# Optimization experiments

Measured on AMD Instinct MI355X. Metric: run time of the kernel, lower is better.

## Reference

```python
import jax, jax.numpy as jnp
import numpy as np

N_SIGMA = 1
K_INST = 8  # instance ids 1..K_INST (0 = background)
W_INST, W_VAR, W_SEED = 1.0, 10.0, 1.0
FG_WEIGHT = 1.0


def make_xym(h, w):
    # torch buffer: linspace(0,2,2048) x / linspace(0,1,1024) y, sliced to [0:h,0:w]
    xm = jnp.linspace(0.0, 2.0, 2048)[:w]
    ym = jnp.linspace(0.0, 1.0, 1024)[:h]
    return jnp.stack([jnp.broadcast_to(xm[None, :], (h, w)),
                      jnp.broadcast_to(ym[:, None], (h, w))], axis=0)  # [2,h,w]


def lovasz_hinge_flat(logits, labels):
    # logits, labels: [N] float (labels in {0,1})
    signs = 2.0 * labels - 1.0
    errors = 1.0 - logits * signs
    order = jnp.argsort(-errors)            # descending sort of errors
    errors_sorted = errors[order]
    gt_sorted = labels[order]
    gts = gt_sorted.sum()
    inter = gts - jnp.cumsum(gt_sorted)
    union = gts + jnp.cumsum(1.0 - gt_sorted)
    jac = 1.0 - inter / union
    grad = jnp.concatenate([jac[:1], jac[1:] - jac[:-1]])
    # torch impl wraps grad in Variable() -> no gradient through grad
    return jnp.dot(jax.nn.relu(errors_sorted), jax.lax.stop_gradient(grad))


def spatial_emb_loss(predictions, instances):
    B, C, T, h, w = predictions.shape
    xym = make_xym(h, w)
    # Faithful to the torch source: due to loop indentation, only the last
    # time step's var/instance/seed losses survive, and obj_count == 1.
    pred = predictions[:, :, T - 1]          # [B,C,h,w]
    inst = instances[:, 0, T - 1]            # [B,h,w] int
    spatial_emb = jnp.tanh(pred[:, 0:2]) + xym[None]   # [B,2,h,w]
    sigma = pred[:, 2:2 + N_SIGMA]                     # [B,1,h,w]
    seed = jax.nn.sigmoid(pred[:, 2 + N_SIGMA])        # [B,h,w]
    npix = float(h * w)

    def per_image(se, sig, sd, ins):
        bg_loss = jnp.sum(jnp.where(ins == 0, sd ** 2, 0.0))

        def per_id(k):
            m = (ins == k).astype(se.dtype)            # [h,w]
            cnt = m.sum()
            safe = jnp.maximum(cnt, 1.0)
            # to_center=True: center of in-mask pixel coordinates
            center = jnp.sum(xym * m[None], axis=(1, 2)) / safe      # [2]
            s_mean = jnp.sum(sig * m[None], axis=(1, 2)) / safe      # [n_sigma]
            var_l = jnp.sum(m[None] * (sig - jax.lax.stop_gradient(s_mean)[:, None, None]) ** 2) / (safe * N_SIGMA)
            s_exp = jnp.exp(s_mean * 10.0)
            dist = jnp.exp(-jnp.sum((se - center[:, None, None]) ** 2 * s_exp[:, None, None], axis=0))  # [h,w]
            inst_l = lovasz_hinge_flat((dist * 2.0 - 1.0).reshape(-1), m.reshape(-1))
            seed_l = FG_WEIGHT * jnp.sum(m * (sd - jax.lax.stop_gradient(dist)) ** 2)
            present = (cnt > 0).astype(se.dtype)       # torch skips absent ids
            return present * var_l, present * inst_l, present * seed_l

        var_l, inst_l, seed_l = jax.vmap(per_id)(jnp.arange(1, K_INST + 1))
        seed_loss = (bg_loss + seed_l.sum()) / npix
        # obj_count == 1 in the original code (incremented once per t-loop)
        return W_INST * inst_l.sum() + W_VAR * var_l.sum() + W_SEED * seed_loss

    per_b = jax.vmap(per_image)(spatial_emb, sigma, seed, inst)
    # torch: loss = loss / b, with b == B-1 after the loop
    return per_b.sum() / (B - 1)


def setup_inputs():
    key = jax.random.key(0)
    k1, k2 = jax.random.split(key)
    B, C, T, H, W = 4, 4, 2, 512, 1024
    predictions = jax.random.normal(k1, (B, C, T, H, W), dtype=jnp.float32)
    instances = jax.random.randint(k2, (B, 1, T, H, W), 0, K_INST + 1, dtype=jnp.int32)
    labels = jnp.zeros((B, 1, T, H, W), dtype=jnp.int32)  # unused by forward
    return {"predictions": predictions, "instances": instances, "labels": labels}


def reference(predictions, instances, labels):
    return spatial_emb_loss(predictions, instances)
```

## Files before the change

kernel.cpp:

```cpp
#include <hip/hip_runtime.h>

#define H 512
#define WID 1024
#define HW (H*WID)
#define B 4
#define K 8
#define NB 1024
#define NBLK1 128

#define OFF_LOSS  0
#define OFF_TICK  1
#define OFF_FIN   16
#define OFF_SPART 512
#define OFF_RED   (OFF_SPART + B*K*NBLK1*8)
#define OFF_PART  (OFF_RED + 2*B*K*NB)

static __device__ __forceinline__ float frcp(float x){
#if __has_builtin(__builtin_amdgcn_rcpf)
  return __builtin_amdgcn_rcpf(x);
#else
  return 1.0f / x;
#endif
}
static __device__ __forceinline__ float fexp2(float x){
#if __has_builtin(__builtin_amdgcn_exp2f)
  return __builtin_amdgcn_exp2f(x);
#else
  return exp2f(x);
#endif
}
static __device__ __forceinline__ float ftanh(float x){
  return 1.0f - 2.0f * frcp(__expf(2.0f*x) + 1.0f);
}
static __device__ __forceinline__ float fsigmoid(float x){
  return frcp(1.0f + __expf(-x));
}

__global__ __launch_bounds__(512) void k1_stats(const float* __restrict__ pred,
                                                const int* __restrict__ inst,
                                                float* __restrict__ ws) {
  const int b = blockIdx.y;
  __shared__ int4   ti[1024];
  __shared__ float4 ts[1024];
  __shared__ float  part5[K][5];
  const float4* sig4 = (const float4*)(pred + (size_t)(8*b + 5) * HW);
  const int4*   ins4 = (const int4*)(inst + (size_t)(2*b + 1) * HW);
  const int base4 = blockIdx.x * 1024;
  #pragma unroll
  for (int i = 0; i < 2; i++) {
    const int q = threadIdx.x + i*512;
    ti[q] = ins4[base4 + q];
    ts[q] = sig4[base4 + q];
  }
  __syncthreads();
  const int wv = threadIdx.x >> 6, lane = threadIdx.x & 63;
  const int kk = wv + 1;
  float cnt=0.f, sx=0.f, sy=0.f, ss=0.f, ss2=0.f;
  #pragma unroll
  for (int j = 0; j < 16; j++) {
    const int q = lane + 64*j;
    const int4   iv = ti[q];
    const float4 sv = ts[q];
    const int p = (base4 + q) * 4;
    const float xm0 = (float)(p & (WID-1)) * (2.0f/2047.0f);
    const float ym  = (float)(p >> 10)     * (1.0f/1023.0f);
    const float m0 = (iv.x==kk)?1.f:0.f, m1=(iv.y==kk)?1.f:0.f,
                m2 = (iv.z==kk)?1.f:0.f, m3=(iv.w==kk)?1.f:0.f;
    const float msum = (m0+m1)+(m2+m3);
    cnt += msum;
    sx  += msum*xm0 + (m1 + 2.0f*m2 + 3.0f*m3)*(2.0f/2047.0f);
    sy  += msum*ym;
    ss  += m0*sv.x + m1*sv.y + m2*sv.z + m3*sv.w;
    ss2 += m0*sv.x*sv.x + m1*sv.y*sv.y + m2*sv.z*sv.z + m3*sv.w*sv.w;
  }
  #pragma unroll
  for (int o=1;o<64;o<<=1){
    cnt+=__shfl_xor(cnt,o,64);
    sx +=__shfl_xor(sx, o,64);
    sy +=__shfl_xor(sy, o,64);
    ss +=__shfl_xor(ss, o,64);
    ss2+=__shfl_xor(ss2,o,64);
  }
  if (lane == 0) {
    part5[wv][0]=cnt; part5[wv][1]=sx; part5[wv][2]=sy; part5[wv][3]=ss; part5[wv][4]=ss2;
  }
  __syncthreads();
  if (threadIdx.x < K*8) {
    const int w = threadIdx.x >> 3, c = threadIdx.x & 7;
    if (c < 5)
      ws[OFF_SPART + ((size_t)(b*K + w)*NBLK1 + blockIdx.x)*8 + c] = part5[w][c];
  }
}

template<int G>
__global__ __launch_bounds__(1024, 8) void k3_main(const float* __restrict__ pred,
                                                   const int* __restrict__ inst,
                                                   float* __restrict__ ws,
                                                   unsigned int* __restrict__ part) {
  const int b = blockIdx.y, g = blockIdx.x;
  __shared__ unsigned int hist[K*NB];
  __shared__ float4 finL[K];
  __shared__ float  vlocL[K];
  for (int i = threadIdx.x*4; i < K*NB; i += 1024*4)
    *(uint4*)&hist[i] = make_uint4(0u,0u,0u,0u);
  const int wv = threadIdx.x >> 6, lane = threadIdx.x & 63;
  if (wv < K) {
    const float* p = ws + OFF_SPART + (size_t)(b*K + wv)*NBLK1*8;
    const float4 q0 = *(const float4*)(p + (size_t)lane*8);
    const float  e0 = p[(size_t)lane*8 + 4];
    const float4 q1 = *(const float4*)(p + (size_t)(lane+64)*8);
    const float  e1 = p[(size_t)(lane+64)*8 + 4];
    float a0=q0.x+q1.x, a1=q0.y+q1.y, a2=q0.z+q1.z, a3=q0.w+q1.w, a4=e0+e1;
    #pragma unroll
    for (int o=1;o<64;o<<=1){
      a0+=__shfl_xor(a0,o,64); a1+=__shfl_xor(a1,o,64); a2+=__shfl_xor(a2,o,64);
      a3+=__shfl_xor(a3,o,64); a4+=__shfl_xor(a4,o,64);
    }
    if (lane == 0) {
      const float cnt=a0, sx=a1, sy=a2, ss=a3, ss2=a4;
      const float present = (cnt > 0.0f) ? 1.0f : 0.0f;
      const float safe = fmaxf(cnt, 1.0f);
      const float cx = sx/safe, cy = sy/safe, sm = ss/safe;
      const float var = (ss2 - 2.0f*sm*ss + sm*sm*cnt)/safe;
      const float sexp = expf(10.0f * sm);
      const float L2E = 1.4426950408889634f;
      finL[wv] = make_float4(-sexp*L2E,
                              2.0f*sexp*cx*L2E,
                              2.0f*sexp*cy*L2E,
                             -sexp*(cx*cx + cy*cy)*L2E + 10.0f);
      vlocL[wv] = present * 10.0f * var * (1.0f/3.0f);
      if (g == 0) ws[OFF_FIN + (b*K + wv)*8 + 4] = cnt;
    }
  }
  __syncthreads();
  float4 fr[K];
  #pragma unroll
  for (int k=0;k<K;k++) fr[k] = finL[k];
  const float4* p0 = (const float4*)(pred + (size_t)(8*b+1)*HW);
  const float4* p1 = (const float4*)(pred + (size_t)(8*b+3)*HW);
  const float4* p3 = (const float4*)(pred + (size_t)(8*b+7)*HW);
  const int4*   in4 = (const int4*)(inst + (size_t)(2*b+1)*HW);
  float sAcc = 0.0f;
  constexpr int CH4 = HW / (G*4);
  const int base4 = g * CH4;
  for (int q0 = 0; q0 < CH4; q0 += 1024) {
    const int idx = base4 + q0 + threadIdx.x;
    const int4   iv = in4[idx];
    const float4 f0 = p0[idx];
    const float4 f1 = p1[idx];
    const float4 f3 = p3[idx];
    const int p = idx * 4;
    const float xm0 = (float)(p & (WID-1)) * (2.0f/2047.0f);
    const float ym  = (float)(p >> 10)     * (1.0f/1023.0f);
    const int ivv[4] = {iv.x, iv.y, iv.z, iv.w};
    float pxv[4], pyv[4], t2v[4], down[4];
    {
      const float a0v[4] = {f0.x, f0.y, f0.z, f0.w};
      const float a1v[4] = {f1.x, f1.y, f1.z, f1.w};
      #pragma unroll
      for (int e=0;e<4;e++){
        pxv[e] = ftanh(a0v[e]) + xm0 + (float)e*(2.0f/2047.0f);
        pyv[e] = ftanh(a1v[e]) + ym;
        t2v[e] = pxv[e]*pxv[e] + pyv[e]*pyv[e];
        down[e] = 0.0f;
      }
    }
    #pragma unroll
    for (int j=0;j<K;j++){
      const float4 f = fr[j];
      int buv[4]; unsigned addv[4];
      #pragma unroll
      for (int e=0;e<4;e++){
        const float u = fmaf(f.x, t2v[e], fmaf(f.y, pxv[e], fmaf(f.z, pyv[e], f.w)));
        const float v = fexp2(u);
        int vi = (int)v; vi = (vi > NB-1) ? NB-1 : vi;
        const bool own = (ivv[e] == j+1);
        if (own) down[e] = v;
        buv[e] = own ? (NB-1 - vi) : vi;
        addv[e] = own ? 0x10001u : 1u;
      }
      int cur = buv[0]; unsigned acc = addv[0];
      #pragma unroll
      for (int e=1;e<4;e++){
        const bool same = (buv[e] == cur);
        if (!same) atomicAdd(&hist[j*NB + cur], acc);
        acc = same ? acc + addv[e] : addv[e];
        cur = buv[e];
      }
      atomicAdd(&hist[j*NB + cur], acc);
    }
    {
      const float sdv[4] = {fsigmoid(f3.x), fsigmoid(f3.y), fsigmoid(f3.z), fsigmoid(f3.w)};
      #pragma unroll
      for (int e=0;e<4;e++){
        const float d  = (ivv[e] == 0) ? 0.0f : down[e] * (1.0f/1024.0f);
        const float df = sdv[e] - d;
        sAcc += df*df;
      }
    }
  }
  __syncthreads();
  unsigned int* dst = part + ((size_t)b*G + g)*(K*NB);
  for (int i = threadIdx.x*4; i < K*NB; i += 1024*4)
    *(uint4*)&dst[i] = *(const uint4*)&hist[i];
  #pragma unroll
  for (int o=1;o<64;o<<=1) sAcc += __shfl_xor(sAcc, o, 64);
  __shared__ float wsum[16];
  if (lane == 0) wsum[wv] = sAcc;
  __syncthreads();
  if (threadIdx.x == 0) {
    float tot = 0.f;
    #pragma unroll
    for (int w = 0; w < 16; w++) tot += wsum[w];
    float add = tot * (1.0f/((float)HW * 3.0f));
    if (g == 0) {
      #pragma unroll
      for (int k = 0; k < K; k++) add += vlocL[k];
    }
    atomicAdd(ws + OFF_LOSS, add);
  }
}

__global__ __launch_bounds__(128) void k4a_reduce(const unsigned int* __restrict__ part,
                                                  unsigned int* __restrict__ red, int G) {
  const int bk = blockIdx.x, c = blockIdx.y;
  const int b = bk >> 3, k = bk & 7;
  const int bu = c*128 + threadIdx.x;
  const unsigned int* base = part + (size_t)b*G*K*NB + (size_t)k*NB + bu;
  unsigned int rc = 0, rp = 0;
  #pragma unroll 8
  for (int g = 0; g < G; g++) {
    const unsigned int v = base[(size_t)g*K*NB];
    rc += v & 0xFFFFu;
    rp += v >> 16;
  }
  red[bk*NB + bu]            = rc;
  red[B*K*NB + bk*NB + bu]   = rp;
}

__global__ __launch_bounds__(256) void k4b_lovasz(const unsigned int* __restrict__ red,
                                                   float* __restrict__ ws,
                                                   float* __restrict__ out) {
  const int bk = blockIdx.x;
  const float cntF = ws[OFF_FIN + bk*8 + 4];
  const int t = threadIdx.x;
  if (cntF > 0.0f) {
    const double Pd = (double)cntF;
    const int lane = t & 63, wv = t >> 6;
    unsigned int cnt[4], pos[4];
    #pragma unroll
    for (int j = 0; j < 4; j++) {
      const int bu = NB-1 - (t*4 + j);
      cnt[j] = red[bk*NB + bu];
      pos[j] = red[B*K*NB + bk*NB + bu];
    }
    const int lc = (int)(cnt[0]+cnt[1]+cnt[2]+cnt[3]);
    const int lp = (int)(pos[0]+pos[1]+pos[2]+pos[3]);
    int ic = lc, ip = lp;
    #pragma unroll
    for (int o=1;o<64;o<<=1){
      const int vc = __shfl_up(ic, o, 64);
      const int vp = __shfl_up(ip, o, 64);
      if (lane >= o) { ic += vc; ip += vp; }
    }
    __shared__ int wtc[4], wtp[4];
    if (lane == 63) { wtc[wv] = ic; wtp[wv] = ip; }
    __syncthreads();
    int offc = 0, offp = 0;
    for (int w = 0; w < wv; w++) { offc += wtc[w]; offp += wtp[w]; }
    int irun = offc + ic - lc;
    int crun = offp + ip - lp;
    double acc = 0.0;
    #pragma unroll
    for (int j = 0; j < 4; j++) {
      const int n = (int)cnt[j];
      if (n) {
        const int bu = NB-1 - (t*4 + j);
        const double jac0 = (irun==0) ? 0.0 : 1.0 - (Pd - crun)/(Pd + irun - crun);
        irun += n; crun += (int)pos[j];
        const double jac1 = 1.0 - (Pd - crun)/(Pd + irun - crun);
        acc += ((bu + 0.5) * (2.0/NB)) * (jac1 - jac0);
      }
    }
    #pragma unroll
    for (int o=1;o<64;o<<=1) acc += __shfl_xor(acc, o, 64);
    __shared__ double racc[4];
    if (lane == 0) racc[wv] = acc;
    __syncthreads();
    if (t == 0) {
      const double tot = racc[0]+racc[1]+racc[2]+racc[3];
      atomicAdd(ws + OFF_LOSS, (float)(tot * (1.0/3.0)));
    }
  }
  if (t == 0) {
    __threadfence();
    unsigned int* wsu = (unsigned int*)ws;
    const unsigned int old = atomicAdd(&wsu[OFF_TICK], 1u);
    if (old == (unsigned)(B*K - 1)) {
      __threadfence();
      out[0] = *((volatile float*)(ws + OFF_LOSS));
    }
  }
}

extern "C" void kernel_launch(void* const* d_in, const int* in_sizes, int n_in,
                              void* d_out, int out_size, void* d_ws, size_t ws_size,
                              hipStream_t stream) {
  const float* pred = (const float*)d_in[0];
  const int*   inst = (const int*)d_in[1];
  float* ws  = (float*)d_ws;
  float* out = (float*)d_out;
  unsigned int* red  = ((unsigned int*)d_ws) + OFF_RED;
  unsigned int* part = ((unsigned int*)d_ws) + OFF_PART;
  int G = 128;
  while (G > 32 && ws_size < ((size_t)OFF_PART + (size_t)B*G*K*NB)*4) G >>= 1;
  hipMemsetAsync(d_ws, 0, 128, stream);
  k1_stats<<<dim3(NBLK1,B), 512, 0, stream>>>(pred, inst, ws);
  if      (G == 128) k3_main<128><<<dim3(128,B), 1024, 0, stream>>>(pred, inst, ws, part);
  else if (G ==  64) k3_main< 64><<<dim3( 64,B), 1024, 0, stream>>>(pred, inst, ws, part);
  else               k3_main< 32><<<dim3( 32,B), 1024, 0, stream>>>(pred, inst, ws, part);
  k4a_reduce<<<dim3(B*K, 8), 128, 0, stream>>>(part, red, G);
  k4b_lovasz<<<B*K, 256, 0, stream>>>(red, ws, out);
}
```

Baseline: 134.0 us.

## Replace per-block histogram dump and reduce kernel with global 64-bit atomics

Each k3 block now adds its shared-memory histogram directly into a global 64-bit count/pos array with atomics, skipping zero bins. This removes the per-block partial-histogram write of about 16 MB and the separate k4a reduce kernel. The memset is folded into k1, which zeros the accumulator, and G is fixed at 128. The cost is contention from global 64-bit atomics across 128 blocks per image.

```diff
diff --git a/kernel.cpp b/kernel.cpp
--- a/kernel.cpp
+++ b/kernel.cpp
@@ -6,6 +6,7 @@
 #define B 4
 #define K 8
 #define NB 1024
+#define G 128
 #define NBLK1 128
 
 #define OFF_LOSS  0
@@ -13,7 +14,6 @@
 #define OFF_FIN   16
 #define OFF_SPART 512
 #define OFF_RED   (OFF_SPART + B*K*NBLK1*8)
-#define OFF_PART  (OFF_RED + 2*B*K*NB)
 
 static __device__ __forceinline__ float frcp(float x){
 #if __has_builtin(__builtin_amdgcn_rcpf)
@@ -38,11 +38,20 @@
 
 __global__ __launch_bounds__(512) void k1_stats(const float* __restrict__ pred,
                                                 const int* __restrict__ inst,
-                                                float* __restrict__ ws) {
+                                                float* __restrict__ ws,
+                                                unsigned long long* __restrict__ red64) {
   const int b = blockIdx.y;
   __shared__ int4   ti[1024];
   __shared__ float4 ts[1024];
   __shared__ float  part5[K][5];
+  {
+    const int blin = b*NBLK1 + blockIdx.x;
+    if (threadIdx.x < 64) red64[(size_t)blin*64 + threadIdx.x] = 0ull;
+    if (blin == 0 && threadIdx.x == 64) {
+      ws[OFF_LOSS] = 0.0f;
+      ((unsigned int*)ws)[OFF_TICK] = 0u;
+    }
+  }
   const float4* sig4 = (const float4*)(pred + (size_t)(8*b + 5) * HW);
   const int4*   ins4 = (const int4*)(inst + (size_t)(2*b + 1) * HW);
   const int base4 = blockIdx.x * 1024;
@@ -92,11 +101,10 @@
   }
 }
 
-template<int G>
 __global__ __launch_bounds__(1024, 8) void k3_main(const float* __restrict__ pred,
                                                    const int* __restrict__ inst,
                                                    float* __restrict__ ws,
-                                                   unsigned int* __restrict__ part) {
+                                                   unsigned long long* __restrict__ red64) {
   const int b = blockIdx.y, g = blockIdx.x;
   __shared__ unsigned int hist[K*NB];
   __shared__ float4 finL[K];
@@ -141,10 +149,8 @@
   const float4* p3 = (const float4*)(pred + (size_t)(8*b+7)*HW);
   const int4*   in4 = (const int4*)(inst + (size_t)(2*b+1)*HW);
   float sAcc = 0.0f;
-  constexpr int CH4 = HW / (G*4);
-  const int base4 = g * CH4;
-  for (int q0 = 0; q0 < CH4; q0 += 1024) {
-    const int idx = base4 + q0 + threadIdx.x;
+  const int idx = g*1024 + threadIdx.x;
+  {
     const int4   iv = in4[idx];
     const float4 f0 = p0[idx];
     const float4 f1 = p1[idx];
@@ -200,9 +206,18 @@
     }
   }
   __syncthreads();
-  unsigned int* dst = part + ((size_t)b*G + g)*(K*NB);
-  for (int i = threadIdx.x*4; i < K*NB; i += 1024*4)
-    *(uint4*)&dst[i] = *(const uint4*)&hist[i];
+  {
+    const size_t rb = (size_t)b * (K*NB);
+    #pragma unroll
+    for (int r = 0; r < 8; r++) {
+      const int i = threadIdx.x + r*1024;
+      const unsigned v = hist[i];
+      if (v)
+        atomicAdd(&red64[rb + i],
+                  (unsigned long long)(v & 0xFFFFu) |
+                  ((unsigned long long)(v >> 16) << 32));
+    }
+  }
   #pragma unroll
   for (int o=1;o<64;o<<=1) sAcc += __shfl_xor(sAcc, o, 64);
   __shared__ float wsum[16];
@@ -221,24 +236,7 @@
   }
 }
 
-__global__ __launch_bounds__(128) void k4a_reduce(const unsigned int* __restrict__ part,
-                                                  unsigned int* __restrict__ red, int G) {
-  const int bk = blockIdx.x, c = blockIdx.y;
-  const int b = bk >> 3, k = bk & 7;
-  const int bu = c*128 + threadIdx.x;
-  const unsigned int* base = part + (size_t)b*G*K*NB + (size_t)k*NB + bu;
-  unsigned int rc = 0, rp = 0;
-  #pragma unroll 8
-  for (int g = 0; g < G; g++) {
-    const unsigned int v = base[(size_t)g*K*NB];
-    rc += v & 0xFFFFu;
-    rp += v >> 16;
-  }
-  red[bk*NB + bu]            = rc;
-  red[B*K*NB + bk*NB + bu]   = rp;
-}
-
-__global__ __launch_bounds__(256) void k4b_lovasz(const unsigned int* __restrict__ red,
+__global__ __launch_bounds__(256) void k4b_lovasz(const unsigned long long* __restrict__ red64,
                                                    float* __restrict__ ws,
                                                    float* __restrict__ out) {
   const int bk = blockIdx.x;
@@ -251,8 +249,9 @@
     #pragma unroll
     for (int j = 0; j < 4; j++) {
       const int bu = NB-1 - (t*4 + j);
-      cnt[j] = red[bk*NB + bu];
-      pos[j] = red[B*K*NB + bk*NB + bu];
+      const unsigned long long vv = red64[(size_t)bk*NB + bu];
+      cnt[j] = (unsigned int)(vv & 0xFFFFFFFFull);
+      pos[j] = (unsigned int)(vv >> 32);
     }
     const int lc = (int)(cnt[0]+cnt[1]+cnt[2]+cnt[3]);
     const int lp = (int)(pos[0]+pos[1]+pos[2]+pos[3]);
@@ -310,15 +309,10 @@
   const int*   inst = (const int*)d_in[1];
   float* ws  = (float*)d_ws;
   float* out = (float*)d_out;
-  unsigned int* red  = ((unsigned int*)d_ws) + OFF_RED;
-  unsigned int* part = ((unsigned int*)d_ws) + OFF_PART;
-  int G = 128;
-  while (G > 32 && ws_size < ((size_t)OFF_PART + (size_t)B*G*K*NB)*4) G >>= 1;
-  hipMemsetAsync(d_ws, 0, 128, stream);
-  k1_stats<<<dim3(NBLK1,B), 512, 0, stream>>>(pred, inst, ws);
-  if      (G == 128) k3_main<128><<<dim3(128,B), 1024, 0, stream>>>(pred, inst, ws, part);
-  else if (G ==  64) k3_main< 64><<<dim3( 64,B), 1024, 0, stream>>>(pred, inst, ws, part);
-  else               k3_main< 32><<<dim3( 32,B), 1024, 0, stream>>>(pred, inst, ws, part);
-  k4a_reduce<<<dim3(B*K, 8), 128, 0, stream>>>(part, red, G);
-  k4b_lovasz<<<B*K, 256, 0, stream>>>(red, ws, out);
-}
+  unsigned long long* red64 =
+      (unsigned long long*)(((unsigned int*)d_ws) + OFF_RED);
+  (void)ws_size;
+  k1_stats  <<<dim3(NBLK1,B), 512, 0, stream>>>(pred, inst, ws, red64);
+  k3_main   <<<dim3(G,B), 1024, 0, stream>>>(pred, inst, ws, red64);
+  k4b_lovasz<<<B*K, 256, 0, stream>>>(red64, ws, out);
+}
```

Result: slower. 142.3 us (+6.2%).

## Fuse histogram reduction into Lovasz kernel and drop workspace memset

Applied to the files above, without the earlier changes.

Merges the separate partial-histogram reduction kernel into the Lovasz scan kernel. Each of the 32 blocks now runs 1024 threads that each reduce one bin across G partials, then scan in-block, so the intermediate red buffer is gone. The hipMemsetAsync is replaced by having k1_stats block 0 zero the loss and tick counters. This removes one launch, one memset and a global round trip, but the reduction now runs on only 32 blocks instead of 256. It also relies on no other k1_stats block needing those counters before k3.

```diff
diff --git a/kernel.cpp b/kernel.cpp
--- a/kernel.cpp
+++ b/kernel.cpp
@@ -12,8 +12,7 @@
 #define OFF_TICK  1
 #define OFF_FIN   16
 #define OFF_SPART 512
-#define OFF_RED   (OFF_SPART + B*K*NBLK1*8)
-#define OFF_PART  (OFF_RED + 2*B*K*NB)
+#define OFF_PART  (OFF_SPART + B*K*NBLK1*8)
 
 static __device__ __forceinline__ float frcp(float x){
 #if __has_builtin(__builtin_amdgcn_rcpf)
@@ -43,6 +42,10 @@
   __shared__ int4   ti[1024];
   __shared__ float4 ts[1024];
   __shared__ float  part5[K][5];
+  if (b == 0 && blockIdx.x == 0) {
+    if (threadIdx.x == 0) ws[OFF_LOSS] = 0.0f;
+    if (threadIdx.x == 1) ((unsigned int*)ws)[OFF_TICK] = 0u;
+  }
   const float4* sig4 = (const float4*)(pred + (size_t)(8*b + 5) * HW);
   const int4*   ins4 = (const int4*)(inst + (size_t)(2*b + 1) * HW);
   const int base4 = blockIdx.x * 1024;
@@ -221,74 +224,54 @@
   }
 }
 
-__global__ __launch_bounds__(128) void k4a_reduce(const unsigned int* __restrict__ part,
-                                                  unsigned int* __restrict__ red, int G) {
-  const int bk = blockIdx.x, c = blockIdx.y;
+__global__ __launch_bounds__(1024) void k4ab_lovasz(const unsigned int* __restrict__ part,
+                                                    float* __restrict__ ws,
+                                                    float* __restrict__ out, int G_) {
+  const int bk = blockIdx.x;
   const int b = bk >> 3, k = bk & 7;
-  const int bu = c*128 + threadIdx.x;
-  const unsigned int* base = part + (size_t)b*G*K*NB + (size_t)k*NB + bu;
-  unsigned int rc = 0, rp = 0;
-  #pragma unroll 8
-  for (int g = 0; g < G; g++) {
-    const unsigned int v = base[(size_t)g*K*NB];
-    rc += v & 0xFFFFu;
-    rp += v >> 16;
-  }
-  red[bk*NB + bu]            = rc;
-  red[B*K*NB + bk*NB + bu]   = rp;
-}
-
-__global__ __launch_bounds__(256) void k4b_lovasz(const unsigned int* __restrict__ red,
-                                                   float* __restrict__ ws,
-                                                   float* __restrict__ out) {
-  const int bk = blockIdx.x;
+  const int t = threadIdx.x, lane = t & 63, wv = t >> 6;
+  __shared__ int    wtc[16], wtp[16];
+  __shared__ double racc[16];
   const float cntF = ws[OFF_FIN + bk*8 + 4];
-  const int t = threadIdx.x;
   if (cntF > 0.0f) {
     const double Pd = (double)cntF;
-    const int lane = t & 63, wv = t >> 6;
-    unsigned int cnt[4], pos[4];
-    #pragma unroll
-    for (int j = 0; j < 4; j++) {
-      const int bu = NB-1 - (t*4 + j);
-      cnt[j] = red[bk*NB + bu];
-      pos[j] = red[B*K*NB + bk*NB + bu];
-    }
-    const int lc = (int)(cnt[0]+cnt[1]+cnt[2]+cnt[3]);
-    const int lp = (int)(pos[0]+pos[1]+pos[2]+pos[3]);
-    int ic = lc, ip = lp;
+    const int bu = NB-1 - t;
+    unsigned rc = 0, rp = 0;
+    const unsigned int* base = part + (size_t)b*G_*(K*NB) + (size_t)k*NB + bu;
+    #pragma unroll 8
+    for (int g = 0; g < G_; g++) {
+      const unsigned v = base[(size_t)g*(K*NB)];
+      rc += v & 0xFFFFu;
+      rp += v >> 16;
+    }
+    int ic = (int)rc, ip = (int)rp;
     #pragma unroll
     for (int o=1;o<64;o<<=1){
       const int vc = __shfl_up(ic, o, 64);
       const int vp = __shfl_up(ip, o, 64);
       if (lane >= o) { ic += vc; ip += vp; }
     }
-    __shared__ int wtc[4], wtp[4];
     if (lane == 63) { wtc[wv] = ic; wtp[wv] = ip; }
     __syncthreads();
     int offc = 0, offp = 0;
     for (int w = 0; w < wv; w++) { offc += wtc[w]; offp += wtp[w]; }
-    int irun = offc + ic - lc;
-    int crun = offp + ip - lp;
+    const int irun = offc + ic - (int)rc;
+    const int crun = offp + ip - (int)rp;
     double acc = 0.0;
-    #pragma unroll
-    for (int j = 0; j < 4; j++) {
-      const int n = (int)cnt[j];
-      if (n) {
-        const int bu = NB-1 - (t*4 + j);
-        const double jac0 = (irun==0) ? 0.0 : 1.0 - (Pd - crun)/(Pd + irun - crun);
-        irun += n; crun += (int)pos[j];
-        const double jac1 = 1.0 - (Pd - crun)/(Pd + irun - crun);
-        acc += ((bu + 0.5) * (2.0/NB)) * (jac1 - jac0);
-      }
+    if (rc) {
+      const double jac0 = (irun==0) ? 0.0 : 1.0 - (Pd - crun)/(Pd + irun - crun);
+      const int ir1 = irun + (int)rc, cr1 = crun + (int)rp;
+      const double jac1 = 1.0 - (Pd - cr1)/(Pd + ir1 - cr1);
+      acc = ((bu + 0.5) * (2.0/NB)) * (jac1 - jac0);
     }
     #pragma unroll
     for (int o=1;o<64;o<<=1) acc += __shfl_xor(acc, o, 64);
-    __shared__ double racc[4];
     if (lane == 0) racc[wv] = acc;
     __syncthreads();
     if (t == 0) {
-      const double tot = racc[0]+racc[1]+racc[2]+racc[3];
+      double tot = 0.0;
+      #pragma unroll
+      for (int w = 0; w < 16; w++) tot += racc[w];
       atomicAdd(ws + OFF_LOSS, (float)(tot * (1.0/3.0)));
     }
   }
@@ -310,15 +293,12 @@
   const int*   inst = (const int*)d_in[1];
   float* ws  = (float*)d_ws;
   float* out = (float*)d_out;
-  unsigned int* red  = ((unsigned int*)d_ws) + OFF_RED;
   unsigned int* part = ((unsigned int*)d_ws) + OFF_PART;
   int G = 128;
   while (G > 32 && ws_size < ((size_t)OFF_PART + (size_t)B*G*K*NB)*4) G >>= 1;
-  hipMemsetAsync(d_ws, 0, 128, stream);
   k1_stats<<<dim3(NBLK1,B), 512, 0, stream>>>(pred, inst, ws);
   if      (G == 128) k3_main<128><<<dim3(128,B), 1024, 0, stream>>>(pred, inst, ws, part);
   else if (G ==  64) k3_main< 64><<<dim3( 64,B), 1024, 0, stream>>>(pred, inst, ws, part);
   else               k3_main< 32><<<dim3( 32,B), 1024, 0, stream>>>(pred, inst, ws, part);
-  k4a_reduce<<<dim3(B*K, 8), 128, 0, stream>>>(part, red, G);
-  k4b_lovasz<<<B*K, 256, 0, stream>>>(red, ws, out);
-}
+  k4ab_lovasz<<<B*K, 1024, 0, stream>>>(part, ws, out, G);
+}
```

Measured after the change: 133.4 us. No clear change (-0.4%).

## Merge histogram atomics across lane quads with DPP and drop memset

Applied to the files above, without the earlier changes.

Before each shared-memory histogram atomic, neighbouring lanes that target the same bin combine their increments with DPP quad permutes, so fewer atomics are issued. The host memset is removed, and k1 now zeroes the loss accumulator and the tick counter itself. OFF_FIN moves to 64 so the finalize area does not overlap that zeroed region. This aims to cut LDS atomic contention and one launch, at the cost of extra permute instructions and a reliance on k1 running before anything reads those slots.

```diff
diff --git a/kernel.cpp b/kernel.cpp
--- a/kernel.cpp
+++ b/kernel.cpp
@@ -10,7 +10,7 @@
 
 #define OFF_LOSS  0
 #define OFF_TICK  1
-#define OFF_FIN   16
+#define OFF_FIN   64
 #define OFF_SPART 512
 #define OFF_RED   (OFF_SPART + B*K*NBLK1*8)
 #define OFF_PART  (OFF_RED + 2*B*K*NB)
@@ -34,6 +34,20 @@
 }
 static __device__ __forceinline__ float fsigmoid(float x){
   return frcp(1.0f + __expf(-x));
+}
+static __device__ __forceinline__ int dpp_xor1_i(int x){
+#if __has_builtin(__builtin_amdgcn_mov_dpp)
+  return __builtin_amdgcn_mov_dpp(x, 0xB1, 0xF, 0xF, true);
+#else
+  return __shfl_xor(x, 1, 64);
+#endif
+}
+static __device__ __forceinline__ int dpp_xor2_i(int x){
+#if __has_builtin(__builtin_amdgcn_mov_dpp)
+  return __builtin_amdgcn_mov_dpp(x, 0x4E, 0xF, 0xF, true);
+#else
+  return __shfl_xor(x, 2, 64);
+#endif
 }
 
 __global__ __launch_bounds__(512) void k1_stats(const float* __restrict__ pred,
@@ -43,6 +57,10 @@
   __shared__ int4   ti[1024];
   __shared__ float4 ts[1024];
   __shared__ float  part5[K][5];
+  if (b == 0 && blockIdx.x == 0) {
+    if (threadIdx.x == 0) ws[OFF_LOSS] = 0.0f;
+    if (threadIdx.x == 1) ((unsigned int*)ws)[OFF_TICK] = 0u;
+  }
   const float4* sig4 = (const float4*)(pred + (size_t)(8*b + 5) * HW);
   const int4*   ins4 = (const int4*)(inst + (size_t)(2*b + 1) * HW);
   const int base4 = blockIdx.x * 1024;
@@ -187,7 +205,15 @@
         acc = same ? acc + addv[e] : addv[e];
         cur = buv[e];
       }
-      atomicAdd(&hist[j*NB + cur], acc);
+      {
+        const int      nb1 = dpp_xor1_i(cur);
+        const unsigned na1 = (unsigned)dpp_xor1_i((int)acc);
+        if (nb1 == cur) acc = (lane & 1) ? 0u : acc + na1;
+        const int      nb2 = dpp_xor2_i(cur);
+        const unsigned na2 = (unsigned)dpp_xor2_i((int)acc);
+        if (nb2 == cur) acc = (lane & 2) ? 0u : acc + na2;
+      }
+      if (acc) atomicAdd(&hist[j*NB + cur], acc);
     }
     {
       const float sdv[4] = {fsigmoid(f3.x), fsigmoid(f3.y), fsigmoid(f3.z), fsigmoid(f3.w)};
@@ -222,15 +248,15 @@
 }
 
 __global__ __launch_bounds__(128) void k4a_reduce(const unsigned int* __restrict__ part,
-                                                  unsigned int* __restrict__ red, int G) {
+                                                  unsigned int* __restrict__ red, int G_) {
   const int bk = blockIdx.x, c = blockIdx.y;
   const int b = bk >> 3, k = bk & 7;
   const int bu = c*128 + threadIdx.x;
-  const unsigned int* base = part + (size_t)b*G*K*NB + (size_t)k*NB + bu;
+  const unsigned int* base = part + (size_t)b*G_*(K*NB) + (size_t)k*NB + bu;
   unsigned int rc = 0, rp = 0;
   #pragma unroll 8
-  for (int g = 0; g < G; g++) {
-    const unsigned int v = base[(size_t)g*K*NB];
+  for (int g = 0; g < G_; g++) {
+    const unsigned int v = base[(size_t)g*(K*NB)];
     rc += v & 0xFFFFu;
     rp += v >> 16;
   }
@@ -314,7 +340,6 @@
   unsigned int* part = ((unsigned int*)d_ws) + OFF_PART;
   int G = 128;
   while (G > 32 && ws_size < ((size_t)OFF_PART + (size_t)B*G*K*NB)*4) G >>= 1;
-  hipMemsetAsync(d_ws, 0, 128, stream);
   k1_stats<<<dim3(NBLK1,B), 512, 0, stream>>>(pred, inst, ws);
   if      (G == 128) k3_main<128><<<dim3(128,B), 1024, 0, stream>>>(pred, inst, ws, part);
   else if (G ==  64) k3_main< 64><<<dim3( 64,B), 1024, 0, stream>>>(pred, inst, ws, part);
```

Measured after the change: 134.7 us. Within noise of the previous version (+0.5%).
